# Performance work log

Hardware: AMD Instinct MI355X
Metric: run time of the kernel (lower is better)

The kernel has to match this reference:

```python
import jax, jax.numpy as jnp
import numpy as np

VOCAB, N_EMBD, BLOCK = 50257, 384, 2048
B, T = 4, 2048


def setup_inputs() -> dict:
    key = jax.random.key(0)
    ks = jax.random.split(key, 9)
    s = 0.02
    return {
        "idx": jax.random.randint(ks[0], (B, T), 0, VOCAB),
        "targets": jax.random.randint(ks[1], (B, T), 0, VOCAB),
        "tok_emb": jax.random.normal(ks[2], (VOCAB, N_EMBD), jnp.float32) * s,
        "pos_emb": jax.random.normal(ks[3], (BLOCK, N_EMBD), jnp.float32) * s,
        "Wk": jax.random.normal(ks[4], (N_EMBD, N_EMBD), jnp.float32) * s,  # stored (in,out)
        "Wq": jax.random.normal(ks[5], (N_EMBD, N_EMBD), jnp.float32) * s,
        "Wv": jax.random.normal(ks[6], (N_EMBD, N_EMBD), jnp.float32) * s,
        "W_head": jax.random.normal(ks[7], (N_EMBD, VOCAB), jnp.float32) * s,
        "b_head": jnp.zeros((VOCAB,), jnp.float32),
    }


def reference(idx, targets, tok_emb, pos_emb, Wk, Wq, Wv, W_head, b_head):
    Bb, Tt = idx.shape
    C = tok_emb.shape[1]
    x = tok_emb[idx] + pos_emb[:Tt]                      # [B,T,C]
    K = x @ Wk
    Q = x @ Wq
    V = x @ Wv
    scores = jnp.einsum('btc,bsc->bts', Q, K) / jnp.sqrt(jnp.float32(C))
    causal = jnp.tril(jnp.ones((Tt, Tt), dtype=bool))
    scores = jnp.where(causal, scores, -jnp.inf)
    weights = jax.nn.softmax(scores, axis=-1)
    out = jnp.einsum('bts,bsc->btc', weights, V)          # [B,T,C]
    logits = out @ W_head + b_head                        # [B,T,V]
    logits2d = logits.reshape(Bb * Tt, -1)
    tgt = targets.reshape(-1)
    logp = jax.nn.log_softmax(logits2d, axis=-1)
    loss = -jnp.mean(jnp.take_along_axis(logp, tgt[:, None], axis=1))
    return (logits2d, loss)
```

## Files before the change

### kernel.cpp

```cpp
#include <hip/hip_runtime.h>
#include <hip/hip_bf16.h>

#define AS1 __attribute__((address_space(1)))
#define AS3 __attribute__((address_space(3)))

typedef __bf16 bf16x8 __attribute__((ext_vector_type(8)));
typedef float  f32x4  __attribute__((ext_vector_type(4)));

__device__ __forceinline__ unsigned short f2b(float f) {
    union { __hip_bfloat16 h; unsigned short u; } v;
    v.h = __float2bfloat16(f);
    return v.u;
}

__device__ __forceinline__ void gload16(const void* g, void* l) {
    __builtin_amdgcn_global_load_lds((AS1 void*)(unsigned long long)g,
                                     (AS3 void*)(unsigned int)(unsigned long long)l,
                                     16, 0, 0);
}

__device__ __forceinline__ void gemm128_core(
    const char* Asrc, int ldaB,
    const char* Bsrc, int ldbB,
    int ksteps,
    unsigned short* lA, unsigned short* lB,
    f32x4 acc[4][4])
{
    const int tid  = threadIdx.x;
    const int wave = tid >> 6;
    const int lane = tid & 63;
    const int wm = wave >> 1, wn = wave & 1;

    const int c0 = 2 * wave, c1 = 2 * wave + 1;
    const int srowl = lane & 15;
    const int skb   = (lane >> 4) * 16;

    const char* a00 = Asrc + (size_t)(c0 * 16 + srowl) * ldaB + skb;
    const char* a10 = Asrc + (size_t)(c1 * 16 + srowl) * ldaB + skb;
    const char* b00 = Bsrc + (size_t)(c0 * 16 + srowl) * ldbB + skb;
    const char* b10 = Bsrc + (size_t)(c1 * 16 + srowl) * ldbB + skb;

#define STAGE(BOFF) do { \
        gload16(a00,      lA + (BOFF) + c0 * 1024); \
        gload16(a00 + 64, lA + (BOFF) + c0 * 1024 + 512); \
        gload16(a10,      lA + (BOFF) + c1 * 1024); \
        gload16(a10 + 64, lA + (BOFF) + c1 * 1024 + 512); \
        gload16(b00,      lB + (BOFF) + c0 * 1024); \
        gload16(b00 + 64, lB + (BOFF) + c0 * 1024 + 512); \
        gload16(b10,      lB + (BOFF) + c1 * 1024); \
        gload16(b10 + 64, lB + (BOFF) + c1 * 1024 + 512); \
        a00 += 128; a10 += 128; b00 += 128; b10 += 128; } while (0)

    STAGE(0);

    for (int ks = 0; ks < ksteps; ++ks) {
        const int cur = ks & 1;
        if (ks + 1 < ksteps) {
            STAGE((cur ^ 1) * 8192);
            asm volatile("s_waitcnt vmcnt(8)" ::: "memory");
        } else {
            asm volatile("s_waitcnt vmcnt(0)" ::: "memory");
        }
        __builtin_amdgcn_sched_barrier(0);
        __builtin_amdgcn_s_barrier();
        __builtin_amdgcn_sched_barrier(0);
        asm volatile("" ::: "memory");

        const unsigned short* rA = lA + cur * 8192;
        const unsigned short* rB = lB + cur * 8192;
        bf16x8 af[4][2], bg[4][2];
#pragma unroll
        for (int m = 0; m < 4; ++m)
#pragma unroll
            for (int kh = 0; kh < 2; ++kh)
                af[m][kh] = *(const bf16x8*)(rA + (wm * 4 + m) * 1024 + kh * 512 + lane * 8);
#pragma unroll
        for (int n = 0; n < 4; ++n)
#pragma unroll
            for (int kh = 0; kh < 2; ++kh)
                bg[n][kh] = *(const bf16x8*)(rB + (wn * 4 + n) * 1024 + kh * 512 + lane * 8);

        __builtin_amdgcn_s_setprio(1);
#pragma unroll
        for (int kh = 0; kh < 2; ++kh)
#pragma unroll
            for (int m = 0; m < 4; ++m)
#pragma unroll
                for (int n = 0; n < 4; ++n)
                    acc[m][n] = __builtin_amdgcn_mfma_f32_16x16x32_bf16(af[m][kh], bg[n][kh], acc[m][n], 0, 0, 0);
        __builtin_amdgcn_s_setprio(0);

        __builtin_amdgcn_sched_barrier(0);
        asm volatile("" ::: "memory");
        __builtin_amdgcn_s_barrier();
        __builtin_amdgcn_sched_barrier(0);
    }
#undef STAGE
}

__global__ __launch_bounds__(384) void k_embed(
    const int* __restrict__ idx, const float* __restrict__ tok,
    const float* __restrict__ pos, unsigned short* __restrict__ xb)
{
    const int i = blockIdx.x;
    const int c = threadIdx.x;
    const int t = i & 2047;
    float v = tok[(size_t)idx[i] * 384 + c] + pos[(size_t)t * 384 + c];
    xb[(size_t)i * 384 + c] = f2b(v);
}

__global__ __launch_bounds__(256) void k_wt_all(
    const float* __restrict__ Wq, const float* __restrict__ Wk,
    const float* __restrict__ Wv, unsigned short* __restrict__ wt)
{
    int gid = blockIdx.x * 256 + threadIdx.x;
    if (gid >= 1152 * 384) return;
    int n = gid / 384, k = gid % 384;
    const float* W; int col;
    if (n < 384)      { W = Wq; col = n; }
    else if (n < 768) { W = Wk; col = n - 384; }
    else              { W = Wv; col = n - 768; }
    wt[gid] = f2b(W[(size_t)k * 384 + col]);
}

__global__ __launch_bounds__(256) void k_wht(
    const float* __restrict__ Wh, unsigned short* __restrict__ wht)
{
    __shared__ unsigned short tile[32][33];
    const int n0 = blockIdx.x * 32, k0 = blockIdx.y * 32;
    const int tx = threadIdx.x, ty = threadIdx.y;
#pragma unroll
    for (int yy = ty; yy < 32; yy += 8) {
        int n = n0 + tx;
        float v = (n < 50257) ? Wh[(size_t)(k0 + yy) * 50257 + n] : 0.f;
        tile[yy][tx] = f2b(v);
    }
    __syncthreads();
#pragma unroll
    for (int yy = ty; yy < 32; yy += 8)
        wht[(size_t)(n0 + yy) * 384 + k0 + tx] = tile[tx][yy];
}

__global__ __launch_bounds__(256) void k_vt(
    const unsigned short* __restrict__ qkv, unsigned short* __restrict__ vt)
{
    __shared__ unsigned short tile[32][33];
    const int t0 = blockIdx.x * 32, c0 = blockIdx.y * 32, b = blockIdx.z;
    const int tx = threadIdx.x, ty = threadIdx.y;
#pragma unroll
    for (int yy = ty; yy < 32; yy += 8)
        tile[yy][tx] = qkv[((size_t)b * 2048 + t0 + yy) * 1152 + 768 + c0 + tx];
    __syncthreads();
#pragma unroll
    for (int yy = ty; yy < 32; yy += 8)
        vt[((size_t)b * 384 + c0 + yy) * 2048 + t0 + tx] = tile[tx][yy];
}

__global__ __launch_bounds__(256) void k_gemm_qkv(
    const unsigned short* __restrict__ xb, const unsigned short* __restrict__ wt,
    unsigned short* __restrict__ qkv)
{
    __shared__ unsigned short lA[16384], lB[16384];
    const int brow = blockIdx.x * 128;
    const int bcol = blockIdx.y * 128;
    f32x4 acc[4][4] = {};
    gemm128_core((const char*)(xb + (size_t)brow * 384), 768,
                 (const char*)(wt + (size_t)bcol * 384), 768, 6, lA, lB, acc);
    const int tid = threadIdx.x, wave = tid >> 6, lane = tid & 63;
    const int wm = wave >> 1, wn = wave & 1, l15 = lane & 15, l4 = lane >> 4;
#pragma unroll
    for (int m = 0; m < 4; ++m)
#pragma unroll
        for (int n = 0; n < 4; ++n)
#pragma unroll
            for (int r = 0; r < 4; ++r) {
                int row = brow + wm * 64 + m * 16 + l4 * 4 + r;
                int col = bcol + wn * 64 + n * 16 + l15;
                qkv[(size_t)row * 1152 + col] = f2b(acc[m][n][r]);
            }
}

__global__ __launch_bounds__(256) void k_gemm_scores(
    const unsigned short* __restrict__ qkv, float* __restrict__ scores)
{
    const int j = blockIdx.x, i = blockIdx.y, b = blockIdx.z;
    if (j > i) return;
    __shared__ unsigned short lA[16384], lB[16384];
    f32x4 acc[4][4] = {};
    const unsigned short* Q = qkv + ((size_t)b * 2048 + i * 128) * 1152;
    const unsigned short* K = qkv + ((size_t)b * 2048 + j * 128) * 1152 + 384;
    gemm128_core((const char*)Q, 2304, (const char*)K, 2304, 6, lA, lB, acc);
    const int tid = threadIdx.x, wave = tid >> 6, lane = tid & 63;
    const int wm = wave >> 1, wn = wave & 1, l15 = lane & 15, l4 = lane >> 4;
    const float sc = 0.0510310363f;
#pragma unroll
    for (int m = 0; m < 4; ++m)
#pragma unroll
        for (int n = 0; n < 4; ++n)
#pragma unroll
            for (int r = 0; r < 4; ++r) {
                int t = i * 128 + wm * 64 + m * 16 + l4 * 4 + r;
                int s = j * 128 + wn * 64 + n * 16 + l15;
                float v = (s <= t) ? acc[m][n][r] * sc : -1e30f;
                scores[((size_t)b * 2048 + t) * 2048 + s] = v;
            }
}

__global__ __launch_bounds__(256) void k_softmax(float* __restrict__ scores)
{
    const int row = blockIdx.x;
    const int t = row & 2047;
    const int Send = ((t >> 7) + 1) << 7;
    const int tid = threadIdx.x, lane = tid & 63, wave = tid >> 6;
    float* srow = scores + (size_t)row * 2048;
    unsigned short* wrow = (unsigned short*)scores + (size_t)row * 4096;

    float vals[8]; int cnt = 0;
    float sum = 0.f;
    for (int s = tid; s < Send; s += 256) {
        float e = __expf(srow[s]);
        vals[cnt++] = e; sum += e;
    }
    __shared__ float red[4];
#pragma unroll
    for (int off = 32; off; off >>= 1) sum += __shfl_xor(sum, off);
    if (lane == 0) red[wave] = sum;
    __syncthreads();
    sum = red[0] + red[1] + red[2] + red[3];

    float inv = 1.f / sum;
    int k2 = 0;
    for (int s = tid; s < Send; s += 256) wrow[s] = f2b(vals[k2++] * inv);
}

__global__ __launch_bounds__(256) void k_gemm_pv(
    const float* __restrict__ scores, const unsigned short* __restrict__ vt,
    unsigned short* __restrict__ outb)
{
    const int x = blockIdx.x;
    const int i = blockIdx.y;
    const int b = blockIdx.z;
    __shared__ unsigned short lA[16384], lB[16384];
    f32x4 acc[4][4] = {};
    const unsigned short* A = (const unsigned short*)scores + ((size_t)b * 2048 + i * 128) * 4096;
    const unsigned short* B = vt + ((size_t)b * 384 + x * 128) * 2048;
    gemm128_core((const char*)A, 8192, (const char*)B, 4096, (i + 1) * 2, lA, lB, acc);
    const int tid = threadIdx.x, wave = tid >> 6, lane = tid & 63;
    const int wm = wave >> 1, wn = wave & 1, l15 = lane & 15, l4 = lane >> 4;
#pragma unroll
    for (int m = 0; m < 4; ++m)
#pragma unroll
        for (int n = 0; n < 4; ++n)
#pragma unroll
            for (int r = 0; r < 4; ++r) {
                int row = b * 2048 + i * 128 + wm * 64 + m * 16 + l4 * 4 + r;
                int col = x * 128 + wn * 64 + n * 16 + l15;
                outb[(size_t)row * 384 + col] = f2b(acc[m][n][r]);
            }
}

__global__ __launch_bounds__(512, 2) void k_gemm_head(
    const unsigned short* __restrict__ outb, const unsigned short* __restrict__ wht,
    const float* __restrict__ bhead, float* __restrict__ logits,
    float* __restrict__ ps)
{
    const int i  = blockIdx.x;
    const int jn = blockIdx.y;
    const int brow = i * 256, bcol = jn * 256;
    __shared__ unsigned short lA[32768], lB[32768];

    const int tid  = threadIdx.x;
    const int wave = tid >> 6;
    const int lane = tid & 63;
    const int wm = wave >> 2;
    const int wn = wave & 3;

    const int c0 = 2 * wave, c1 = 2 * wave + 1;
    const int srowl = lane & 15;
    const int skb   = (lane >> 4) * 16;

    const char* Asrc = (const char*)(outb + (size_t)brow * 384);
    const char* Bsrc = (const char*)(wht + (size_t)bcol * 384);

    const char* a0 = Asrc + (size_t)(c0 * 16 + srowl) * 768 + skb;
    const char* a1 = Asrc + (size_t)(c1 * 16 + srowl) * 768 + skb;
    const char* b0 = Bsrc + (size_t)(c0 * 16 + srowl) * 768 + skb;
    const char* b1 = Bsrc + (size_t)(c1 * 16 + srowl) * 768 + skb;

    f32x4 acc[8][4] = {};

#define STAGE6(BOFF) do { \
        gload16(a0,      lA + (BOFF) + c0 * 1024); \
        gload16(a0 + 64, lA + (BOFF) + c0 * 1024 + 512); \
        gload16(a1,      lA + (BOFF) + c1 * 1024); \
        gload16(a1 + 64, lA + (BOFF) + c1 * 1024 + 512); \
        gload16(b0,      lB + (BOFF) + c0 * 1024); \
        gload16(b0 + 64, lB + (BOFF) + c0 * 1024 + 512); \
        gload16(b1,      lB + (BOFF) + c1 * 1024); \
        gload16(b1 + 64, lB + (BOFF) + c1 * 1024 + 512); \
        a0 += 128; a1 += 128; b0 += 128; b1 += 128; } while (0)

    STAGE6(0);

#pragma unroll 1
    for (int ks = 0; ks < 6; ++ks) {
        const int cur = ks & 1;
        if (ks < 5) {
            STAGE6((cur ^ 1) * 16384);
            asm volatile("s_waitcnt vmcnt(8)" ::: "memory");
        } else {
            asm volatile("s_waitcnt vmcnt(0)" ::: "memory");
        }
        __builtin_amdgcn_sched_barrier(0);
        __builtin_amdgcn_s_barrier();
        __builtin_amdgcn_sched_barrier(0);
        asm volatile("" ::: "memory");

        const unsigned short* rA = lA + cur * 16384;
        const unsigned short* rB = lB + cur * 16384;
#pragma unroll
        for (int kh = 0; kh < 2; ++kh) {
            bf16x8 af[8], bg[4];
#pragma unroll
            for (int m = 0; m < 8; ++m)
                af[m] = *(const bf16x8*)(rA + (wm * 8 + m) * 1024 + kh * 512 + lane * 8);
#pragma unroll
            for (int n = 0; n < 4; ++n)
                bg[n] = *(const bf16x8*)(rB + (wn * 4 + n) * 1024 + kh * 512 + lane * 8);
            __builtin_amdgcn_s_setprio(1);
#pragma unroll
            for (int m = 0; m < 8; ++m)
#pragma unroll
                for (int n = 0; n < 4; ++n)
                    acc[m][n] = __builtin_amdgcn_mfma_f32_16x16x32_bf16(af[m], bg[n], acc[m][n], 0, 0, 0);
            __builtin_amdgcn_s_setprio(0);
        }
        __builtin_amdgcn_sched_barrier(0);
        asm volatile("" ::: "memory");
        __builtin_amdgcn_s_barrier();
        __builtin_amdgcn_sched_barrier(0);
    }
#undef STAGE6

    const int l15 = lane & 15, l4 = lane >> 4;
    float bv[4]; int cv[4]; bool ok[4];
#pragma unroll
    for (int n = 0; n < 4; ++n) {
        int c = bcol + wn * 64 + n * 16 + l15;
        cv[n] = c;
        ok[n] = (c < 50257);
        bv[n] = ok[n] ? bhead[c] : 0.f;
    }

    float (*part)[64] = (float(*)[64])lA;
#pragma unroll
    for (int m = 0; m < 8; ++m) {
#pragma unroll
        for (int r = 0; r < 4; ++r) {
            int pr = wm * 128 + m * 16 + l4 * 4 + r;
            size_t grow = (size_t)(brow + pr);
            float s = 0.f;
#pragma unroll
            for (int n = 0; n < 4; ++n) {
                float x = acc[m][n][r] + bv[n];
                if (ok[n]) {
                    logits[grow * 50257 + cv[n]] = x;
                    s += __expf(x);
                }
            }
            part[pr][((wn * 16 + l15) + pr) & 63] = s;
        }
    }
    __syncthreads();
    if (tid < 256) {
        float S = 0.f;
#pragma unroll 8
        for (int j = 0; j < 64; ++j) S += part[tid][(j + tid) & 63];
        ps[(size_t)(brow + tid) * 197 + jn] = S;
    }
}

__global__ __launch_bounds__(256) void k_loss_row(
    const float* __restrict__ ps, const float* __restrict__ logits,
    const int* __restrict__ targets, float* __restrict__ rowloss)
{
    const int tid = threadIdx.x;
    const int row = blockIdx.x * 4 + (tid >> 6);
    const int lane = tid & 63;
    float s = 0.f;
    for (int nb = lane; nb < 197; nb += 64) s += ps[(size_t)row * 197 + nb];
#pragma unroll
    for (int off = 32; off; off >>= 1) s += __shfl_xor(s, off);
    if (lane == 0) {
        float lse = logf(s);
        int tg = targets[row];
        float lt = logits[(size_t)row * 50257 + tg];
        rowloss[row] = lse - lt;
    }
}

__global__ __launch_bounds__(256) void k_loss_final(
    const float* __restrict__ rowloss, float* __restrict__ out_loss)
{
    const int tid = threadIdx.x;
    float s = 0.f;
    for (int r = tid; r < 8192; r += 256) s += rowloss[r];
    __shared__ float red2[256];
    red2[tid] = s;
    __syncthreads();
    for (int off = 128; off; off >>= 1) {
        if (tid < off) red2[tid] += red2[tid + off];
        __syncthreads();
    }
    if (tid == 0) out_loss[0] = red2[0] * (1.0f / 8192.0f);
}

extern "C" void kernel_launch(void* const* d_in, const int* in_sizes, int n_in,
                              void* d_out, int out_size, void* d_ws, size_t ws_size,
                              hipStream_t stream)
{
    (void)in_sizes; (void)n_in; (void)out_size; (void)ws_size;
    const int*   idx = (const int*)d_in[0];
    const int*   tgt = (const int*)d_in[1];
    const float* tok = (const float*)d_in[2];
    const float* pos = (const float*)d_in[3];
    const float* Wk  = (const float*)d_in[4];
    const float* Wq  = (const float*)d_in[5];
    const float* Wv  = (const float*)d_in[6];
    const float* Wh  = (const float*)d_in[7];
    const float* bh  = (const float*)d_in[8];

    float* logits = (float*)d_out;
    float* loss   = logits + (size_t)8192 * 50257;

    char* ws = (char*)d_ws;
    unsigned short* xb   = (unsigned short*)(ws + 0);
    unsigned short* wt   = (unsigned short*)(ws + 6291456);
    unsigned short* qkv  = (unsigned short*)(ws + 7176192);
    unsigned short* vt   = (unsigned short*)(ws + 26050560);
    unsigned short* outb = (unsigned short*)(ws + 32342016);
    unsigned short* wht  = (unsigned short*)(ws + 38633472);
    float* scores        = (float*)(ws + 77365248);
    float* psb           = (float*)(ws + 144474112);
    float* rl            = (float*)(ws + 150929408);

    k_embed      <<<dim3(8192),       dim3(384),   0, stream>>>(idx, tok, pos, xb);
    k_wt_all     <<<dim3(1728),       dim3(256),   0, stream>>>(Wq, Wk, Wv, wt);
    k_wht        <<<dim3(1576, 12),   dim3(32, 8), 0, stream>>>(Wh, wht);
    k_gemm_qkv   <<<dim3(64, 9),      dim3(256),   0, stream>>>(xb, wt, qkv);
    k_vt         <<<dim3(64, 12, 4),  dim3(32, 8), 0, stream>>>(qkv, vt);
    k_gemm_scores<<<dim3(16, 16, 4),  dim3(256),   0, stream>>>(qkv, scores);
    k_softmax    <<<dim3(8192),       dim3(256),   0, stream>>>(scores);
    k_gemm_pv    <<<dim3(3, 16, 4),   dim3(256),   0, stream>>>(scores, vt, outb);
    k_gemm_head  <<<dim3(32, 197),    dim3(512),   0, stream>>>(outb, wht, bh, logits, psb);
    k_loss_row   <<<dim3(2048),       dim3(256),   0, stream>>>(psb, logits, tgt, rl);
    k_loss_final <<<dim3(1),          dim3(256),   0, stream>>>(rl, loss);
}
```

Baseline: 1.047 ms.

## Interleave head GEMM loads with MFMA in fine-grained four-phase ping-pong schedule

After: 1.046 ms. Within noise of the previous version (-0.0%).

```diff
diff --git a/kernel.cpp b/kernel.cpp
--- a/kernel.cpp
+++ b/kernel.cpp
@@ -17,6 +17,14 @@
     __builtin_amdgcn_global_load_lds((AS1 void*)(unsigned long long)g,
                                      (AS3 void*)(unsigned int)(unsigned long long)l,
                                      16, 0, 0);
+}
+
+__device__ __forceinline__ void block_sync() {
+    __builtin_amdgcn_sched_barrier(0);
+    asm volatile("" ::: "memory");
+    __builtin_amdgcn_s_barrier();
+    asm volatile("" ::: "memory");
+    __builtin_amdgcn_sched_barrier(0);
 }
 
 __device__ __forceinline__ void gemm128_core(
@@ -289,58 +297,109 @@
 
     f32x4 acc[8][4] = {};
 
-#define STAGE6(BOFF) do { \
-        gload16(a0,      lA + (BOFF) + c0 * 1024); \
-        gload16(a0 + 64, lA + (BOFF) + c0 * 1024 + 512); \
-        gload16(a1,      lA + (BOFF) + c1 * 1024); \
-        gload16(a1 + 64, lA + (BOFF) + c1 * 1024 + 512); \
-        gload16(b0,      lB + (BOFF) + c0 * 1024); \
-        gload16(b0 + 64, lB + (BOFF) + c0 * 1024 + 512); \
-        gload16(b1,      lB + (BOFF) + c1 * 1024); \
-        gload16(b1 + 64, lB + (BOFF) + c1 * 1024 + 512); \
-        a0 += 128; a1 += 128; b0 += 128; b1 += 128; } while (0)
-
-    STAGE6(0);
+    {
+        char* dA = (char*)lA; char* dB = (char*)lB;
+        gload16(b0,      dB + c0 * 2048);
+        gload16(b1,      dB + c1 * 2048);
+        gload16(a0,      dA + c0 * 2048);
+        gload16(a1,      dA + c1 * 2048);
+        gload16(a0 + 64, dA + c0 * 2048 + 1024);
+        gload16(a1 + 64, dA + c1 * 2048 + 1024);
+        gload16(b0 + 64, dB + c0 * 2048 + 1024);
+        gload16(b1 + 64, dB + c1 * 2048 + 1024);
+        a0 += 128; a1 += 128; b0 += 128; b1 += 128;
+    }
+    asm volatile("s_waitcnt vmcnt(4)" ::: "memory");
+    block_sync();
+
+#define LDA4(mh, kh) do { \
+        const char* _p = rA + ((wm * 8 + (mh) * 4) * 2048 + (kh) * 1024) + lane * 16; \
+        af[0] = *(const bf16x8*)(_p); \
+        af[1] = *(const bf16x8*)(_p + 2048); \
+        af[2] = *(const bf16x8*)(_p + 4096); \
+        af[3] = *(const bf16x8*)(_p + 6144); } while (0)
+#define LDB4(kh) do { \
+        const char* _p = rB + ((wn * 4) * 2048 + (kh) * 1024) + lane * 16; \
+        bg[0] = *(const bf16x8*)(_p); \
+        bg[1] = *(const bf16x8*)(_p + 2048); \
+        bg[2] = *(const bf16x8*)(_p + 4096); \
+        bg[3] = *(const bf16x8*)(_p + 6144); } while (0)
+#define MFMA16(mh) do { \
+        __builtin_amdgcn_s_setprio(1); \
+        _Pragma("unroll") \
+        for (int _m = 0; _m < 4; ++_m) \
+            _Pragma("unroll") \
+            for (int _n = 0; _n < 4; ++_n) \
+                acc[(mh) * 4 + _m][_n] = __builtin_amdgcn_mfma_f32_16x16x32_bf16( \
+                    af[_m], bg[_n], acc[(mh) * 4 + _m][_n], 0, 0, 0); \
+        __builtin_amdgcn_s_setprio(0); } while (0)
 
 #pragma unroll 1
-    for (int ks = 0; ks < 6; ++ks) {
-        const int cur = ks & 1;
-        if (ks < 5) {
-            STAGE6((cur ^ 1) * 16384);
-            asm volatile("s_waitcnt vmcnt(8)" ::: "memory");
-        } else {
-            asm volatile("s_waitcnt vmcnt(0)" ::: "memory");
-        }
-        __builtin_amdgcn_sched_barrier(0);
-        __builtin_amdgcn_s_barrier();
-        __builtin_amdgcn_sched_barrier(0);
-        asm volatile("" ::: "memory");
-
-        const unsigned short* rA = lA + cur * 16384;
-        const unsigned short* rB = lB + cur * 16384;
-#pragma unroll
-        for (int kh = 0; kh < 2; ++kh) {
-            bf16x8 af[8], bg[4];
-#pragma unroll
-            for (int m = 0; m < 8; ++m)
-                af[m] = *(const bf16x8*)(rA + (wm * 8 + m) * 1024 + kh * 512 + lane * 8);
-#pragma unroll
-            for (int n = 0; n < 4; ++n)
-                bg[n] = *(const bf16x8*)(rB + (wn * 4 + n) * 1024 + kh * 512 + lane * 8);
-            __builtin_amdgcn_s_setprio(1);
-#pragma unroll
-            for (int m = 0; m < 8; ++m)
-#pragma unroll
-                for (int n = 0; n < 4; ++n)
-                    acc[m][n] = __builtin_amdgcn_mfma_f32_16x16x32_bf16(af[m], bg[n], acc[m][n], 0, 0, 0);
-            __builtin_amdgcn_s_setprio(0);
-        }
-        __builtin_amdgcn_sched_barrier(0);
-        asm volatile("" ::: "memory");
-        __builtin_amdgcn_s_barrier();
-        __builtin_amdgcn_sched_barrier(0);
-    }
-#undef STAGE6
+    for (int t = 0; t < 5; ++t) {
+        const int cur = t & 1;
+        const char* rA = (const char*)lA + cur * 32768;
+        const char* rB = (const char*)lB + cur * 32768;
+        char* sA = (char*)lA + (cur ^ 1) * 32768;
+        char* sB = (char*)lB + (cur ^ 1) * 32768;
+        bf16x8 af[4], bg[4];
+
+        LDB4(0); LDA4(0, 0);
+        gload16(b0, sB + c0 * 2048); gload16(b1, sB + c1 * 2048);
+        block_sync();
+        MFMA16(0);
+        block_sync();
+
+        LDA4(1, 0);
+        gload16(a0, sA + c0 * 2048); gload16(a1, sA + c1 * 2048);
+        asm volatile("s_waitcnt vmcnt(4)" ::: "memory");
+        block_sync();
+        MFMA16(1);
+        block_sync();
+
+        LDB4(1); LDA4(0, 1);
+        gload16(a0 + 64, sA + c0 * 2048 + 1024); gload16(a1 + 64, sA + c1 * 2048 + 1024);
+        block_sync();
+        MFMA16(0);
+        block_sync();
+
+        LDA4(1, 1);
+        gload16(b0 + 64, sB + c0 * 2048 + 1024); gload16(b1 + 64, sB + c1 * 2048 + 1024);
+        asm volatile("s_waitcnt vmcnt(4)" ::: "memory");
+        block_sync();
+        MFMA16(1);
+        block_sync();
+
+        a0 += 128; a1 += 128; b0 += 128; b1 += 128;
+    }
+    {
+        const char* rA = (const char*)lA + 32768;
+        const char* rB = (const char*)lB + 32768;
+        bf16x8 af[4], bg[4];
+
+        LDB4(0); LDA4(0, 0);
+        block_sync();
+        MFMA16(0);
+        block_sync();
+
+        LDA4(1, 0);
+        asm volatile("s_waitcnt vmcnt(0)" ::: "memory");
+        block_sync();
+        MFMA16(1);
+        block_sync();
+
+        LDB4(1); LDA4(0, 1);
+        block_sync();
+        MFMA16(0);
+        block_sync();
+
+        LDA4(1, 1);
+        block_sync();
+        MFMA16(1);
+        block_sync();
+    }
+#undef LDA4
+#undef LDB4
+#undef MFMA16
 
     const int l15 = lane & 15, l4 = lane >> 4;
     float bv[4]; int cv[4]; bool ok[4];
```
